# Performance work log

Hardware: AMD Instinct MI355X
Metric: run time of the kernel (lower is better)

Reference implementation:

```python
import jax, jax.numpy as jnp
import numpy as np

C = 256
NH = 8
G = 32  # groupnorm groups (min(32, C))
EPS = 1e-6


def setup_inputs() -> dict:
    key = jax.random.key(0)
    ks = jax.random.split(key, 7)
    B, D, H, W = 2, 16, 16, 16
    x = jax.random.normal(ks[0], (B, C, D, H, W), dtype=jnp.float32)
    gn_gamma = jnp.ones((C,), jnp.float32)
    gn_beta = jnp.zeros((C,), jnp.float32)
    s = 1.0 / np.sqrt(C)
    qkv_w = jax.random.normal(ks[1], (3 * C, C), jnp.float32) * s  # 1x1x1 conv weight
    qkv_b = jnp.zeros((3 * C,), jnp.float32)
    proj_w = jax.random.normal(ks[2], (C, C), jnp.float32) * s
    proj_b = jnp.zeros((C,), jnp.float32)
    return {"x": x, "gn_gamma": gn_gamma, "gn_beta": gn_beta,
            "qkv_w": qkv_w, "qkv_b": qkv_b, "proj_w": proj_w, "proj_b": proj_b}


def _group_norm(x, gamma, beta):
    # x: [B, C, S]
    B, Cc, S = x.shape
    xg = x.reshape(B, G, (Cc // G) * S)
    mu = xg.mean(axis=-1, keepdims=True)
    var = xg.var(axis=-1, keepdims=True)
    xg = (xg - mu) * jax.lax.rsqrt(var + EPS)
    x = xg.reshape(B, Cc, S)
    return x * gamma[None, :, None] + beta[None, :, None]


def reference(x, gn_gamma, gn_beta, qkv_w, qkv_b, proj_w, proj_b):
    B, Cc, D, H, W = x.shape
    S = D * H * W
    hd = Cc // NH
    xf = x.reshape(B, Cc, S)
    h = _group_norm(xf, gn_gamma, gn_beta)
    # 1x1x1 conv == channel matmul: [B, 3C, S]
    qkv = jnp.einsum('oc,bcs->bos', qkv_w, h) + qkv_b[None, :, None]
    # torch path: reshape(B,3C,S).permute(0,2,1).chunk -> q=channels[0:C]
    q, k, v = qkv[:, :Cc], qkv[:, Cc:2 * Cc], qkv[:, 2 * Cc:]
    # [B, C, S] -> [B, NH, S, hd]
    def to_heads(t):
        return t.reshape(B, NH, hd, S).transpose(0, 1, 3, 2)
    q, k, v = to_heads(q), to_heads(k), to_heads(v)
    scale = hd ** (-0.5)
    attn = jax.nn.softmax(jnp.einsum('bnqd,bnkd->bnqk', q, k) * scale, axis=-1)
    o = jnp.einsum('bnqk,bnkd->bnqd', attn, v)  # [B, NH, S, hd]
    o = o.transpose(0, 1, 3, 2).reshape(B, Cc, S)  # back to [B, C, S]
    o = jnp.einsum('oc,bcs->bos', proj_w, o) + proj_b[None, :, None]
    return x + o.reshape(B, Cc, D, H, W)
```

## Files before the change

### kernel.cpp

```cpp
#include <hip/hip_runtime.h>
#include <cstddef>

#define S_LEN 4096
#define C_DIM 256
#define NHEADS 8
#define HDIM 32

typedef __attribute__((ext_vector_type(8))) _Float16 half8;
typedef __attribute__((ext_vector_type(4))) _Float16 half4;
typedef __attribute__((ext_vector_type(2))) _Float16 h2t;
typedef __attribute__((ext_vector_type(2))) __fp16 fp16x2;
typedef __attribute__((ext_vector_type(4))) float floatx4;

#define SC2F ((float)(0.17677669529663687 * 1.4426950408889634))

__global__ __launch_bounds__(256) void prep_stats(
    const float* __restrict__ qkv_w, const float* __restrict__ proj_w,
    const float* __restrict__ qkv_b, const float* __restrict__ x,
    _Float16* __restrict__ wq, _Float16* __restrict__ wp,
    float* __restrict__ qbias, float* __restrict__ gstat)
{
  const int blk = blockIdx.x;
  const int tid = threadIdx.x;
  if (blk < 64) {
    __shared__ float red[2][4];
    const int g = blk & 31, b = blk >> 5;
    const float* xb = x + ((size_t)b * C_DIM + g * 8) * S_LEN;
    const float4* x4 = (const float4*)xb;
    float sum = 0.f, sumsq = 0.f;
    for (int i = tid; i < 8192; i += 256) {
      float4 v = x4[i];
      sum += v.x + v.y + v.z + v.w;
      sumsq += v.x * v.x + v.y * v.y + v.z * v.z + v.w * v.w;
    }
    for (int off = 1; off < 64; off <<= 1) {
      sum += __shfl_xor(sum, off, 64);
      sumsq += __shfl_xor(sumsq, off, 64);
    }
    const int wv = tid >> 6, lane = tid & 63;
    if (lane == 0) { red[0][wv] = sum; red[1][wv] = sumsq; }
    __syncthreads();
    if (tid == 0) {
      float s = red[0][0] + red[0][1] + red[0][2] + red[0][3];
      float sq = red[1][0] + red[1][1] + red[1][2] + red[1][3];
      float mean = s * (1.f / 32768.f);
      float var = sq * (1.f / 32768.f) - mean * mean;
      gstat[((size_t)b * 32 + g) * 2 + 0] = mean;
      gstat[((size_t)b * 32 + g) * 2 + 1] = rsqrtf(var + 1e-6f);
    }
  } else {
    int idx = (blk - 64) * 256 + tid;
    if (idx < 768 * 256) {
      float v = qkv_w[idx];
      if (idx < 256 * 256) v *= SC2F;
      wq[idx] = (_Float16)v;
    } else if (idx < 768 * 256 + 256 * 256) {
      int i = idx - 768 * 256;
      wp[i] = (_Float16)proj_w[i];
    } else if (idx < 768 * 256 + 256 * 256 + 768) {
      int i = idx - (768 * 256 + 256 * 256);
      float bv = qkv_b[i];
      if (i < 256) bv *= SC2F;
      qbias[i] = bv;
    }
  }
}

__global__ __launch_bounds__(256) void qkv_gn_gemm(
    const _Float16* __restrict__ W, const float* __restrict__ bias,
    const float* __restrict__ x, const float* __restrict__ gamma,
    const float* __restrict__ beta, const float* __restrict__ gstat,
    _Float16* __restrict__ qo, _Float16* __restrict__ ko_,
    _Float16* __restrict__ vo)
{
  __shared__ __align__(16) _Float16 Ld[64 * 264];
  const int tid = threadIdx.x;
  const int b = blockIdx.z;
  const int s0 = blockIdx.y * 64;

  {
    const int c0 = (tid & 127) * 2, c1 = c0 + 1;
    const int sh = tid >> 7;
    const int g = c0 >> 3;
    const float mean = gstat[((size_t)b * 32 + g) * 2 + 0];
    const float rstd = gstat[((size_t)b * 32 + g) * 2 + 1];
    const float ga0 = gamma[c0] * rstd, be0 = beta[c0] - mean * ga0;
    const float ga1 = gamma[c1] * rstd, be1 = beta[c1] - mean * ga1;
    const float4* xa = (const float4*)(x + ((size_t)b * C_DIM + c0) * S_LEN + s0 + sh * 32);
    const float4* xc = (const float4*)(x + ((size_t)b * C_DIM + c1) * S_LEN + s0 + sh * 32);
    #pragma unroll
    for (int j = 0; j < 8; ++j) {
      float4 a = xa[j], c = xc[j];
      int sl = sh * 32 + j * 4;
      *(h2t*)&Ld[(sl + 0) * 264 + c0] = (h2t){ (_Float16)(a.x * ga0 + be0), (_Float16)(c.x * ga1 + be1) };
      *(h2t*)&Ld[(sl + 1) * 264 + c0] = (h2t){ (_Float16)(a.y * ga0 + be0), (_Float16)(c.y * ga1 + be1) };
      *(h2t*)&Ld[(sl + 2) * 264 + c0] = (h2t){ (_Float16)(a.z * ga0 + be0), (_Float16)(c.z * ga1 + be1) };
      *(h2t*)&Ld[(sl + 3) * 264 + c0] = (h2t){ (_Float16)(a.w * ga0 + be0), (_Float16)(c.w * ga1 + be1) };
    }
  }
  __syncthreads();

  const int lane = tid & 63, wv = tid >> 6;
  const int m = lane & 15, quad = lane >> 4;
  const int mtb = blockIdx.x * 8 + wv * 2;
  const _Float16* wrow0 = W + (size_t)((mtb + 0) * 16 + m) * C_DIM + quad * 8;
  const _Float16* wrow1 = W + (size_t)((mtb + 1) * 16 + m) * C_DIM + quad * 8;
  const _Float16* lp = &Ld[m * 264 + quad * 8];

  floatx4 acc[2][4];
  #pragma unroll
  for (int j = 0; j < 2; ++j)
    #pragma unroll
    for (int s = 0; s < 4; ++s) acc[j][s] = (floatx4){0.f,0.f,0.f,0.f};

  #pragma unroll
  for (int k0 = 0; k0 < C_DIM; k0 += 32) {
    half8 b0 = *(const half8*)(lp + k0);
    half8 b1 = *(const half8*)(lp + 16 * 264 + k0);
    half8 b2 = *(const half8*)(lp + 32 * 264 + k0);
    half8 b3 = *(const half8*)(lp + 48 * 264 + k0);
    half8 a0 = *(const half8*)(wrow0 + k0);
    half8 a1 = *(const half8*)(wrow1 + k0);
    acc[0][0] = __builtin_amdgcn_mfma_f32_16x16x32_f16(a0, b0, acc[0][0], 0, 0, 0);
    acc[0][1] = __builtin_amdgcn_mfma_f32_16x16x32_f16(a0, b1, acc[0][1], 0, 0, 0);
    acc[0][2] = __builtin_amdgcn_mfma_f32_16x16x32_f16(a0, b2, acc[0][2], 0, 0, 0);
    acc[0][3] = __builtin_amdgcn_mfma_f32_16x16x32_f16(a0, b3, acc[0][3], 0, 0, 0);
    acc[1][0] = __builtin_amdgcn_mfma_f32_16x16x32_f16(a1, b0, acc[1][0], 0, 0, 0);
    acc[1][1] = __builtin_amdgcn_mfma_f32_16x16x32_f16(a1, b1, acc[1][1], 0, 0, 0);
    acc[1][2] = __builtin_amdgcn_mfma_f32_16x16x32_f16(a1, b2, acc[1][2], 0, 0, 0);
    acc[1][3] = __builtin_amdgcn_mfma_f32_16x16x32_f16(a1, b3, acc[1][3], 0, 0, 0);
  }

  #pragma unroll
  for (int j = 0; j < 2; ++j) {
    const int ob = (mtb + j) * 16 + quad * 4;
    const float bv0 = bias[ob], bv1 = bias[ob + 1],
                bv2 = bias[ob + 2], bv3 = bias[ob + 3];
    #pragma unroll
    for (int sub = 0; sub < 4; ++sub) {
      int s = s0 + sub * 16 + m;
      float v0 = acc[j][sub][0] + bv0, v1 = acc[j][sub][1] + bv1,
            v2 = acc[j][sub][2] + bv2, v3 = acc[j][sub][3] + bv3;
      if (ob < 512) {
        _Float16* dst = (ob < 256) ? qo : ko_;
        int oo = ob & 255, n = oo >> 5, d0 = oo & 31;
        half4 h = { (_Float16)v0, (_Float16)v1, (_Float16)v2, (_Float16)v3 };
        *(half4*)(dst + (((size_t)b * NHEADS + n) * S_LEN + s) * HDIM + d0) = h;
      } else {
        int oo = ob - 512, n = oo >> 5, d0 = oo & 31;
        _Float16* dst = vo + ((size_t)b * NHEADS + n) * HDIM * S_LEN + s;
        dst[(size_t)(d0 + 0) * S_LEN] = (_Float16)v0;
        dst[(size_t)(d0 + 1) * S_LEN] = (_Float16)v1;
        dst[(size_t)(d0 + 2) * S_LEN] = (_Float16)v2;
        dst[(size_t)(d0 + 3) * S_LEN] = (_Float16)v3;
      }
    }
  }
}

__global__ __launch_bounds__(512) void attn_kernel(
    const _Float16* __restrict__ q, const _Float16* __restrict__ k,
    const _Float16* __restrict__ v, _Float16* __restrict__ po,
    float* __restrict__ pl)
{
  __shared__ __align__(16) _Float16 Kl[2][64 * 40];
  __shared__ __align__(16) _Float16 Vl[2][32 * 68];
  const int tid = threadIdx.x;
  const int lane = tid & 63, wv = tid >> 6;
  const int m = lane & 15, quad = lane >> 4;
  const int n = blockIdx.y, b = blockIdx.z;
  const int qc = blockIdx.x >> 1, kh = blockIdx.x & 1;
  const int q0 = qc * 128 + wv * 16;
  const int bh = b * NHEADS + n;

  const _Float16* qb = q + (size_t)bh * S_LEN * HDIM;
  const _Float16* kb = k + (size_t)bh * S_LEN * HDIM + (size_t)kh * 2048 * HDIM;
  const _Float16* vb = v + (size_t)bh * HDIM * S_LEN + (size_t)kh * 2048;

  half8 qf = *(const half8*)(qb + (size_t)(q0 + m) * HDIM + quad * 8);

  const int krow = wv * 8 + (lane >> 3), kc = (lane & 7) * 4;
  const int vrow = wv * 4 + (lane >> 4), vc = (lane & 15) * 4;
  const _Float16* kg = kb + (size_t)krow * HDIM + kc;
  const _Float16* vg = vb + (size_t)vrow * S_LEN + vc;
  const int klds = krow * 40 + kc;
  const int vlds = vrow * 68 + vc;

  int2 kreg = *(const int2*)kg;
  int2 vreg = *(const int2*)vg;
  const _Float16* kgp = kg + 64 * HDIM;
  const _Float16* vgp = vg + 64;

  floatx4 o0 = {0.f,0.f,0.f,0.f}, o1 = o0;
  float l0 = 0.f;
  const fp16x2 one2 = { (__fp16)1.0f, (__fp16)1.0f };

  #pragma unroll 2
  for (int it = 0; it < 32; ++it) {
    const int bufi = it & 1;
    *(int2*)(&Kl[bufi][klds]) = kreg;
    *(int2*)(&Vl[bufi][vlds]) = vreg;
    kreg = *(const int2*)kgp; kgp += 64 * HDIM;
    vreg = *(const int2*)vgp; vgp += 64;
    __syncthreads();
    const _Float16* Kb = Kl[bufi];
    const _Float16* Vb = Vl[bufi];
    #pragma unroll
    for (int t = 0; t < 4; ++t) {
      half8 kf = *(const half8*)(Kb + (t * 16 + m) * 40 + quad * 8);
      half4 vf0 = *(const half4*)(Vb + m * 68 + t * 16 + quad * 4);
      half4 vf1 = *(const half4*)(Vb + (16 + m) * 68 + t * 16 + quad * 4);
      floatx4 z = {0.f,0.f,0.f,0.f};
      floatx4 s0 = __builtin_amdgcn_mfma_f32_16x16x32_f16(kf, qf, z, 0, 0, 0);
      float e0 = __builtin_amdgcn_exp2f(s0[0]);
      float e1 = __builtin_amdgcn_exp2f(s0[1]);
      float e2 = __builtin_amdgcn_exp2f(s0[2]);
      float e3 = __builtin_amdgcn_exp2f(s0[3]);
      half4 p0;
      fp16x2 plo = __builtin_amdgcn_cvt_pkrtz(e0, e1);
      fp16x2 phi = __builtin_amdgcn_cvt_pkrtz(e2, e3);
      *(fp16x2*)&p0 = plo;
      *((fp16x2*)&p0 + 1) = phi;
      l0 = __builtin_amdgcn_fdot2(plo, one2, l0, false);
      l0 = __builtin_amdgcn_fdot2(phi, one2, l0, false);
      o0 = __builtin_amdgcn_mfma_f32_16x16x16f16(vf0, p0, o0, 0, 0, 0);
      o1 = __builtin_amdgcn_mfma_f32_16x16x16f16(vf1, p0, o1, 0, 0, 0);
    }
  }
  l0 += __shfl_xor(l0, 16, 64);
  l0 += __shfl_xor(l0, 32, 64);
  _Float16* poh = po + (size_t)kh * 2097152 + ((size_t)bh * S_LEN + q0 + m) * HDIM;
  half4 h0 = { (_Float16)o0[0], (_Float16)o0[1], (_Float16)o0[2], (_Float16)o0[3] };
  half4 h1 = { (_Float16)o1[0], (_Float16)o1[1], (_Float16)o1[2], (_Float16)o1[3] };
  *(half4*)(poh + quad * 4) = h0;
  *(half4*)(poh + 16 + quad * 4) = h1;
  if (quad == 0) pl[(size_t)kh * 65536 + (size_t)bh * S_LEN + q0 + m] = l0;
}

__global__ __launch_bounds__(256) void attn_merge(
    const _Float16* __restrict__ po, const float* __restrict__ pl,
    _Float16* __restrict__ o_t)
{
  const int tid = threadIdx.x;
  const int row = blockIdx.x * 64 + (tid >> 2);
  const int d0 = (tid & 3) * 8;
  const int bh = row >> 12, qq = row & 4095;
  const int b = bh >> 3, n = bh & 7;
  const float l = pl[row] + pl[65536 + row];
  const float inv = 1.f / l;
  half8 a = *(const half8*)(po + (size_t)row * HDIM + d0);
  half8 c = *(const half8*)(po + 2097152 + (size_t)row * HDIM + d0);
  half8 o;
  #pragma unroll
  for (int i = 0; i < 8; ++i)
    o[i] = (_Float16)(((float)a[i] + (float)c[i]) * inv);
  *(half8*)(o_t + ((size_t)b * S_LEN + qq) * C_DIM + n * HDIM + d0) = o;
}

__global__ __launch_bounds__(256) void proj_gemm(
    const _Float16* __restrict__ W, const float* __restrict__ bias,
    const _Float16* __restrict__ o_t, const float* __restrict__ x,
    float* __restrict__ out)
{
  const int tid = threadIdx.x;
  const int lane = tid & 63, wv = tid >> 6;
  const int m = lane & 15, quad = lane >> 4;
  const int mt = blockIdx.x * 4 + wv;
  const int s0 = blockIdx.y * 64;
  const int b = blockIdx.z;
  const int row = mt * 16 + m;
  const _Float16* ob = o_t + (size_t)b * S_LEN * C_DIM;

  const _Float16* wrow = W + (size_t)row * C_DIM + quad * 8;
  const _Float16* h0 = ob + (size_t)(s0 + m) * C_DIM + quad * 8;
  const _Float16* h1 = h0 + 16 * C_DIM;
  const _Float16* h2 = h0 + 32 * C_DIM;
  const _Float16* h3 = h0 + 48 * C_DIM;

  floatx4 acc0 = {0.f,0.f,0.f,0.f}, acc1 = acc0, acc2 = acc0, acc3 = acc0;
  half8 af = *(const half8*)wrow;
  half8 b0 = *(const half8*)h0;
  half8 b1 = *(const half8*)h1;
  half8 b2 = *(const half8*)h2;
  half8 b3 = *(const half8*)h3;
  #pragma unroll
  for (int k0 = 0; k0 < C_DIM; k0 += 32) {
    half8 afn, b0n, b1n, b2n, b3n;
    if (k0 < C_DIM - 32) {
      afn = *(const half8*)(wrow + k0 + 32);
      b0n = *(const half8*)(h0 + k0 + 32);
      b1n = *(const half8*)(h1 + k0 + 32);
      b2n = *(const half8*)(h2 + k0 + 32);
      b3n = *(const half8*)(h3 + k0 + 32);
    }
    acc0 = __builtin_amdgcn_mfma_f32_16x16x32_f16(af, b0, acc0, 0, 0, 0);
    acc1 = __builtin_amdgcn_mfma_f32_16x16x32_f16(af, b1, acc1, 0, 0, 0);
    acc2 = __builtin_amdgcn_mfma_f32_16x16x32_f16(af, b2, acc2, 0, 0, 0);
    acc3 = __builtin_amdgcn_mfma_f32_16x16x32_f16(af, b3, acc3, 0, 0, 0);
    af = afn; b0 = b0n; b1 = b1n; b2 = b2n; b3 = b3n;
  }
  floatx4 accs[4] = {acc0, acc1, acc2, acc3};
  #pragma unroll
  for (int sub = 0; sub < 4; ++sub) {
    int s = s0 + sub * 16 + m;
    #pragma unroll
    for (int r = 0; r < 4; ++r) {
      int c = mt * 16 + quad * 4 + r;
      size_t idx = ((size_t)b * C_DIM + c) * S_LEN + s;
      out[idx] = x[idx] + accs[sub][r] + bias[c];
    }
  }
}

extern "C" void kernel_launch(void* const* d_in, const int* in_sizes, int n_in,
                              void* d_out, int out_size, void* d_ws, size_t ws_size,
                              hipStream_t stream) {
  const float* x        = (const float*)d_in[0];
  const float* gn_gamma = (const float*)d_in[1];
  const float* gn_beta  = (const float*)d_in[2];
  const float* qkv_w    = (const float*)d_in[3];
  const float* qkv_b    = (const float*)d_in[4];
  const float* proj_w   = (const float*)d_in[5];
  const float* proj_b   = (const float*)d_in[6];
  float* out = (float*)d_out;

  const size_t n1 = (size_t)2 * S_LEN * C_DIM;
  char* ws = (char*)d_ws;
  _Float16* o_t = (_Float16*)ws;
  _Float16* qx  = o_t + n1;
  _Float16* kx  = qx + n1;
  _Float16* vx  = kx + n1;
  _Float16* wq  = vx + n1;
  _Float16* wp  = wq + 768 * 256;
  float*    qbias = (float*)(wp + 256 * 256);
  float*    gstat = qbias + 768;
  _Float16* po  = (_Float16*)(gstat + 128);
  float*    pl  = (float*)(po + 2 * n1);

  prep_stats<<<1091, 256, 0, stream>>>(qkv_w, proj_w, qkv_b, x, wq, wp, qbias, gstat);
  qkv_gn_gemm<<<dim3(6, 64, 2), 256, 0, stream>>>(wq, qbias, x, gn_gamma, gn_beta, gstat, qx, kx, vx);
  attn_kernel<<<dim3(64, 8, 2), 512, 0, stream>>>(qx, kx, vx, po, pl);
  attn_merge<<<1024, 256, 0, stream>>>(po, pl, o_t);
  proj_gemm<<<dim3(4, 64, 2), 256, 0, stream>>>(wp, proj_b, o_t, x, out);
}
```

Measured before the change: 166.1 us.

## Fuse split-K attention merge into projection GEMM and widen K/V tiles

The separate merge kernel is removed. The projection GEMM now reads both partial attention outputs and row sums directly, normalises them in fp16, and feeds the result to the MFMAs, which removes one launch and the intermediate o_t round trip through memory. The attention kernel also stages 128 keys per iteration with 16-byte loads instead of 64 keys with 8-byte loads, halving the number of barriers. The cost is more LDS per block, redundant partial loads and reciprocals across the four proj_gemm column blocks, and normalisation now done in fp16 rather than fp32.

Result: slower. 171.1 us (+3.0%).

```diff
diff --git a/kernel.cpp b/kernel.cpp
--- a/kernel.cpp
+++ b/kernel.cpp
@@ -163,8 +163,8 @@
     const _Float16* __restrict__ v, _Float16* __restrict__ po,
     float* __restrict__ pl)
 {
-  __shared__ __align__(16) _Float16 Kl[2][64 * 40];
-  __shared__ __align__(16) _Float16 Vl[2][32 * 68];
+  __shared__ __align__(16) _Float16 Kl[2][128 * 40];
+  __shared__ __align__(16) _Float16 Vl[2][32 * 136];
   const int tid = threadIdx.x;
   const int lane = tid & 63, wv = tid >> 6;
   const int m = lane & 15, quad = lane >> 4;
@@ -179,37 +179,37 @@
 
   half8 qf = *(const half8*)(qb + (size_t)(q0 + m) * HDIM + quad * 8);
 
-  const int krow = wv * 8 + (lane >> 3), kc = (lane & 7) * 4;
-  const int vrow = wv * 4 + (lane >> 4), vc = (lane & 15) * 4;
+  const int krow = tid >> 2, kc = (tid & 3) * 8;
+  const int vrow = tid >> 4, vc = (tid & 15) * 8;
   const _Float16* kg = kb + (size_t)krow * HDIM + kc;
   const _Float16* vg = vb + (size_t)vrow * S_LEN + vc;
   const int klds = krow * 40 + kc;
-  const int vlds = vrow * 68 + vc;
-
-  int2 kreg = *(const int2*)kg;
-  int2 vreg = *(const int2*)vg;
-  const _Float16* kgp = kg + 64 * HDIM;
-  const _Float16* vgp = vg + 64;
+  const int vlds = vrow * 136 + vc;
+
+  int4 kreg = *(const int4*)kg;
+  int4 vreg = *(const int4*)vg;
+  const _Float16* kgp = kg + 128 * HDIM;
+  const _Float16* vgp = vg + 128;
 
   floatx4 o0 = {0.f,0.f,0.f,0.f}, o1 = o0;
   float l0 = 0.f;
   const fp16x2 one2 = { (__fp16)1.0f, (__fp16)1.0f };
 
   #pragma unroll 2
-  for (int it = 0; it < 32; ++it) {
+  for (int it = 0; it < 16; ++it) {
     const int bufi = it & 1;
-    *(int2*)(&Kl[bufi][klds]) = kreg;
-    *(int2*)(&Vl[bufi][vlds]) = vreg;
-    kreg = *(const int2*)kgp; kgp += 64 * HDIM;
-    vreg = *(const int2*)vgp; vgp += 64;
+    *(int4*)(&Kl[bufi][klds]) = kreg;
+    *(int4*)(&Vl[bufi][vlds]) = vreg;
+    kreg = *(const int4*)kgp; kgp += 128 * HDIM;
+    vreg = *(const int4*)vgp; vgp += 128;
     __syncthreads();
     const _Float16* Kb = Kl[bufi];
     const _Float16* Vb = Vl[bufi];
     #pragma unroll
-    for (int t = 0; t < 4; ++t) {
+    for (int t = 0; t < 8; ++t) {
       half8 kf = *(const half8*)(Kb + (t * 16 + m) * 40 + quad * 8);
-      half4 vf0 = *(const half4*)(Vb + m * 68 + t * 16 + quad * 4);
-      half4 vf1 = *(const half4*)(Vb + (16 + m) * 68 + t * 16 + quad * 4);
+      half4 vf0 = *(const half4*)(Vb + m * 136 + t * 16 + quad * 4);
+      half4 vf1 = *(const half4*)(Vb + (16 + m) * 136 + t * 16 + quad * 4);
       floatx4 z = {0.f,0.f,0.f,0.f};
       floatx4 s0 = __builtin_amdgcn_mfma_f32_16x16x32_f16(kf, qf, z, 0, 0, 0);
       float e0 = __builtin_amdgcn_exp2f(s0[0]);
@@ -237,30 +237,10 @@
   if (quad == 0) pl[(size_t)kh * 65536 + (size_t)bh * S_LEN + q0 + m] = l0;
 }
 
-__global__ __launch_bounds__(256) void attn_merge(
-    const _Float16* __restrict__ po, const float* __restrict__ pl,
-    _Float16* __restrict__ o_t)
-{
-  const int tid = threadIdx.x;
-  const int row = blockIdx.x * 64 + (tid >> 2);
-  const int d0 = (tid & 3) * 8;
-  const int bh = row >> 12, qq = row & 4095;
-  const int b = bh >> 3, n = bh & 7;
-  const float l = pl[row] + pl[65536 + row];
-  const float inv = 1.f / l;
-  half8 a = *(const half8*)(po + (size_t)row * HDIM + d0);
-  half8 c = *(const half8*)(po + 2097152 + (size_t)row * HDIM + d0);
-  half8 o;
-  #pragma unroll
-  for (int i = 0; i < 8; ++i)
-    o[i] = (_Float16)(((float)a[i] + (float)c[i]) * inv);
-  *(half8*)(o_t + ((size_t)b * S_LEN + qq) * C_DIM + n * HDIM + d0) = o;
-}
-
 __global__ __launch_bounds__(256) void proj_gemm(
     const _Float16* __restrict__ W, const float* __restrict__ bias,
-    const _Float16* __restrict__ o_t, const float* __restrict__ x,
-    float* __restrict__ out)
+    const _Float16* __restrict__ po, const float* __restrict__ pl,
+    const float* __restrict__ x, float* __restrict__ out)
 {
   const int tid = threadIdx.x;
   const int lane = tid & 63, wv = tid >> 6;
@@ -269,35 +249,37 @@
   const int s0 = blockIdx.y * 64;
   const int b = blockIdx.z;
   const int row = mt * 16 + m;
-  const _Float16* ob = o_t + (size_t)b * S_LEN * C_DIM;
+
+  float inv[8][4];
+  #pragma unroll
+  for (int n = 0; n < 8; ++n) {
+    #pragma unroll
+    for (int sub = 0; sub < 4; ++sub) {
+      size_t idx = ((size_t)(b * NHEADS + n)) * S_LEN + s0 + sub * 16 + m;
+      inv[n][sub] = 1.f / (pl[idx] + pl[65536 + idx]);
+    }
+  }
 
   const _Float16* wrow = W + (size_t)row * C_DIM + quad * 8;
-  const _Float16* h0 = ob + (size_t)(s0 + m) * C_DIM + quad * 8;
-  const _Float16* h1 = h0 + 16 * C_DIM;
-  const _Float16* h2 = h0 + 32 * C_DIM;
-  const _Float16* h3 = h0 + 48 * C_DIM;
-
   floatx4 acc0 = {0.f,0.f,0.f,0.f}, acc1 = acc0, acc2 = acc0, acc3 = acc0;
-  half8 af = *(const half8*)wrow;
-  half8 b0 = *(const half8*)h0;
-  half8 b1 = *(const half8*)h1;
-  half8 b2 = *(const half8*)h2;
-  half8 b3 = *(const half8*)h3;
   #pragma unroll
   for (int k0 = 0; k0 < C_DIM; k0 += 32) {
-    half8 afn, b0n, b1n, b2n, b3n;
-    if (k0 < C_DIM - 32) {
-      afn = *(const half8*)(wrow + k0 + 32);
-      b0n = *(const half8*)(h0 + k0 + 32);
-      b1n = *(const half8*)(h1 + k0 + 32);
-      b2n = *(const half8*)(h2 + k0 + 32);
-      b3n = *(const half8*)(h3 + k0 + 32);
-    }
-    acc0 = __builtin_amdgcn_mfma_f32_16x16x32_f16(af, b0, acc0, 0, 0, 0);
-    acc1 = __builtin_amdgcn_mfma_f32_16x16x32_f16(af, b1, acc1, 0, 0, 0);
-    acc2 = __builtin_amdgcn_mfma_f32_16x16x32_f16(af, b2, acc2, 0, 0, 0);
-    acc3 = __builtin_amdgcn_mfma_f32_16x16x32_f16(af, b3, acc3, 0, 0, 0);
-    af = afn; b0 = b0n; b1 = b1n; b2 = b2n; b3 = b3n;
+    const int n = k0 >> 5;
+    const int d0 = quad * 8;
+    half8 bf[4];
+    #pragma unroll
+    for (int sub = 0; sub < 4; ++sub) {
+      size_t idx = (((size_t)(b * NHEADS + n)) * S_LEN + s0 + sub * 16 + m) * HDIM + d0;
+      half8 a = *(const half8*)(po + idx);
+      half8 c = *(const half8*)(po + 2097152 + idx);
+      _Float16 iv = (_Float16)inv[n][sub];
+      bf[sub] = (a + c) * iv;
+    }
+    half8 af = *(const half8*)(wrow + k0);
+    acc0 = __builtin_amdgcn_mfma_f32_16x16x32_f16(af, bf[0], acc0, 0, 0, 0);
+    acc1 = __builtin_amdgcn_mfma_f32_16x16x32_f16(af, bf[1], acc1, 0, 0, 0);
+    acc2 = __builtin_amdgcn_mfma_f32_16x16x32_f16(af, bf[2], acc2, 0, 0, 0);
+    acc3 = __builtin_amdgcn_mfma_f32_16x16x32_f16(af, bf[3], acc3, 0, 0, 0);
   }
   floatx4 accs[4] = {acc0, acc1, acc2, acc3};
   #pragma unroll
@@ -326,8 +308,7 @@
 
   const size_t n1 = (size_t)2 * S_LEN * C_DIM;
   char* ws = (char*)d_ws;
-  _Float16* o_t = (_Float16*)ws;
-  _Float16* qx  = o_t + n1;
+  _Float16* qx  = (_Float16*)ws;
   _Float16* kx  = qx + n1;
   _Float16* vx  = kx + n1;
   _Float16* wq  = vx + n1;
@@ -340,6 +321,5 @@
   prep_stats<<<1091, 256, 0, stream>>>(qkv_w, proj_w, qkv_b, x, wq, wp, qbias, gstat);
   qkv_gn_gemm<<<dim3(6, 64, 2), 256, 0, stream>>>(wq, qbias, x, gn_gamma, gn_beta, gstat, qx, kx, vx);
   attn_kernel<<<dim3(64, 8, 2), 512, 0, stream>>>(qx, kx, vx, po, pl);
-  attn_merge<<<1024, 256, 0, stream>>>(po, pl, o_t);
-  proj_gemm<<<dim3(4, 64, 2), 256, 0, stream>>>(wp, proj_b, o_t, x, out);
-}
+  proj_gemm<<<dim3(4, 64, 2), 256, 0, stream>>>(wp, proj_b, po, pl, x, out);
+}
```
